# Performance work log

Measured on AMD Instinct MI355X. Metric: run time of the kernel, lower is better.

The kernel has to match this reference:

```python
import jax, jax.numpy as jnp
import numpy as np

EPS = 1e-8


def kabsch_align(P, Q):
    """Align P to Q per the original torch code. P, Q: [B, N, 3].

    Note: the torch code unpacks torch.linalg.svd as (U, S, V) where the third
    return is actually Vh; we faithfully reproduce that exact math.
    """
    P_mean = jnp.mean(P, axis=1, keepdims=True)          # [B,1,3]
    Q_mean = jnp.mean(Q, axis=1, keepdims=True)
    P_c = P - P_mean
    Q_c = Q - Q_mean
    H = jnp.einsum('bni,bnj->bij', P_c, Q_c)             # [B,3,3] covariance
    U, S, Vh = jnp.linalg.svd(H, full_matrices=False)
    Ut = jnp.swapaxes(U, 1, 2)
    d = jnp.linalg.det(jnp.matmul(Vh, Ut))               # [B]
    e = jnp.stack([jnp.ones_like(d), jnp.ones_like(d), d], axis=-1)  # diag(1,1,d)
    R = jnp.einsum('bik,bk,bkj->bij', Vh, e, Ut)         # [B,3,3]
    # P_aligned = P_c @ R^T + Q_mean
    return jnp.einsum('bni,bji->bnj', P_c, R) + Q_mean


def setup_inputs() -> dict:
    key = jax.random.key(0)
    k1, k2 = jax.random.split(key)
    B, K, N = 256, 5, 4096
    preds = jax.random.normal(k1, (B, K, N, 3), dtype=jnp.float32)
    target = jax.random.normal(k2, (B, N, 3), dtype=jnp.float32)
    return {"preds": preds, "target": target}


def reference(preds, target):
    B, K, N, _ = preds.shape
    P = preds.reshape(B * K, N, 3)
    Q = jnp.broadcast_to(target[:, None], (B, K, N, 3)).reshape(B * K, N, 3)
    aligned = kabsch_align(P, Q)                         # [B*K, N, 3]
    mse = jnp.mean((aligned - Q) ** 2, axis=(1, 2))      # [B*K]
    rmsd = jnp.sqrt(mse + EPS).reshape(B, K)
    return jnp.mean(jnp.min(rmsd, axis=1))
```

## Files before the change

kernel.cpp:

```cpp
#include <hip/hip_runtime.h>
#include <math.h>

#define B_    256
#define K_    5
#define N_    4096
#define NPAIR (B_ * K_)
#define NMOM  17

__global__ __launch_bounds__(256) void kabsch_moments(
    const float* __restrict__ preds, const float* __restrict__ target,
    float* __restrict__ mout) {
  const int idx = blockIdx.x;
  const int b = idx & 255;
  const int k = idx >> 8;
  const int pair_orig = b * K_ + k;
  const int tid = threadIdx.x;

  const float4* __restrict__ P4 =
      reinterpret_cast<const float4*>(preds) + (size_t)pair_orig * (N_ * 3 / 4);
  const float4* __restrict__ Q4 =
      reinterpret_cast<const float4*>(target) + (size_t)b * (N_ * 3 / 4);

  float acc[NMOM];
#pragma unroll
  for (int i = 0; i < NMOM; ++i) acc[i] = 0.f;

#pragma unroll
  for (int j = 0; j < 4; ++j) {
    const int c = tid + j * 256;
    const float4 a0 = P4[3 * c + 0], a1 = P4[3 * c + 1], a2 = P4[3 * c + 2];
    const float4 b0 = Q4[3 * c + 0], b1 = Q4[3 * c + 1], b2 = Q4[3 * c + 2];
    const float p[4][3] = {{a0.x, a0.y, a0.z},
                           {a0.w, a1.x, a1.y},
                           {a1.z, a1.w, a2.x},
                           {a2.y, a2.z, a2.w}};
    const float q[4][3] = {{b0.x, b0.y, b0.z},
                           {b0.w, b1.x, b1.y},
                           {b1.z, b1.w, b2.x},
                           {b2.y, b2.z, b2.w}};
#pragma unroll
    for (int m = 0; m < 4; ++m) {
      const float px = p[m][0], py = p[m][1], pz = p[m][2];
      const float qx = q[m][0], qy = q[m][1], qz = q[m][2];
      acc[0] += px; acc[1] += py; acc[2] += pz;
      acc[3] += qx; acc[4] += qy; acc[5] += qz;
      acc[6] = fmaf(px, px, fmaf(py, py, fmaf(pz, pz, acc[6])));
      acc[7] = fmaf(qx, qx, fmaf(qy, qy, fmaf(qz, qz, acc[7])));
      acc[8]  = fmaf(px, qx, acc[8]);
      acc[9]  = fmaf(px, qy, acc[9]);
      acc[10] = fmaf(px, qz, acc[10]);
      acc[11] = fmaf(py, qx, acc[11]);
      acc[12] = fmaf(py, qy, acc[12]);
      acc[13] = fmaf(py, qz, acc[13]);
      acc[14] = fmaf(pz, qx, acc[14]);
      acc[15] = fmaf(pz, qy, acc[15]);
      acc[16] = fmaf(pz, qz, acc[16]);
    }
  }

#pragma unroll
  for (int off = 32; off > 0; off >>= 1) {
#pragma unroll
    for (int i = 0; i < NMOM; ++i) acc[i] += __shfl_down(acc[i], off, 64);
  }

  __shared__ float red[4][NMOM];
  const int lane = tid & 63, wid = tid >> 6;
  if (lane == 0) {
#pragma unroll
    for (int i = 0; i < NMOM; ++i) red[wid][i] = acc[i];
  }
  __syncthreads();
  if (tid < NMOM) {
    mout[(size_t)idx * NMOM + tid] =
        red[0][tid] + red[1][tid] + red[2][tid] + red[3][tid];
  }
}

__device__ inline void cross3(const double* a, const double* b, double* c) {
  c[0] = a[1] * b[2] - a[2] * b[1];
  c[1] = a[2] * b[0] - a[0] * b[2];
  c[2] = a[0] * b[1] - a[1] * b[0];
}
__device__ inline double dot3(const double* a, const double* b) {
  return a[0] * b[0] + a[1] * b[1] + a[2] * b[2];
}
__device__ inline void fixsign3(double* v) {
  const double a0 = fabs(v[0]), a1 = fabs(v[1]), a2 = fabs(v[2]);
  const int i = (a0 >= a1 && a0 >= a2) ? 0 : ((a1 >= a2) ? 1 : 2);
  if (v[i] < 0.0) { v[0] = -v[0]; v[1] = -v[1]; v[2] = -v[2]; }
}
__device__ inline void eigvec3(const double A[3][3], double lam, double* v) {
  const double r0[3] = {A[0][0] - lam, A[0][1], A[0][2]};
  const double r1[3] = {A[1][0], A[1][1] - lam, A[1][2]};
  const double r2[3] = {A[2][0], A[2][1], A[2][2] - lam};
  double c01[3], c02[3], c12[3];
  cross3(r0, r1, c01); cross3(r0, r2, c02); cross3(r1, r2, c12);
  const double n01 = dot3(c01, c01), n02 = dot3(c02, c02), n12 = dot3(c12, c12);
  const double* best = c01; double nb = n01;
  if (n02 > nb) { best = c02; nb = n02; }
  if (n12 > nb) { best = c12; nb = n12; }
  if (nb < 1e-280) { v[0] = 1.0; v[1] = 0.0; v[2] = 0.0; return; }
  const double inv = 1.0 / sqrt(nb);
  v[0] = best[0] * inv; v[1] = best[1] * inv; v[2] = best[2] * inv;
}

__global__ __launch_bounds__(256) void kabsch_svd(
    const float* __restrict__ mo, float* __restrict__ rmsd) {
  const int idx = blockIdx.x * blockDim.x + threadIdx.x;
  if (idx >= NPAIR) return;
  const float* m = mo + (size_t)idx * NMOM;
  const double invN = 1.0 / (double)N_;

  const double sP[3] = {m[0], m[1], m[2]};
  const double sQ[3] = {m[3], m[4], m[5]};
  double H[3][3];
#pragma unroll
  for (int i = 0; i < 3; ++i)
#pragma unroll
    for (int j = 0; j < 3; ++j)
      H[i][j] = (double)m[8 + 3 * i + j] - sP[i] * sQ[j] * invN;

  const double Sp = (double)m[6] - dot3(sP, sP) * invN;
  const double Sq = (double)m[7] - dot3(sQ, sQ) * invN;

  double A[3][3];
#pragma unroll
  for (int i = 0; i < 3; ++i)
#pragma unroll
    for (int j = 0; j < 3; ++j)
      A[i][j] = H[0][i] * H[0][j] + H[1][i] * H[1][j] + H[2][i] * H[2][j];

  double lam[3];
  double V[3][3];
  const double q = (A[0][0] + A[1][1] + A[2][2]) / 3.0;
  const double p1 = A[0][1] * A[0][1] + A[0][2] * A[0][2] + A[1][2] * A[1][2];
  const double p2 = (A[0][0] - q) * (A[0][0] - q) +
                    (A[1][1] - q) * (A[1][1] - q) +
                    (A[2][2] - q) * (A[2][2] - q) + 2.0 * p1;
  if (p2 < 1e-30) {
    lam[0] = lam[1] = lam[2] = q;
#pragma unroll
    for (int i = 0; i < 3; ++i)
#pragma unroll
      for (int j = 0; j < 3; ++j) V[i][j] = (i == j) ? 1.0 : 0.0;
  } else {
    const double p = sqrt(p2 / 6.0);
    const double invp = 1.0 / p;
    double Bm[3][3];
#pragma unroll
    for (int i = 0; i < 3; ++i)
#pragma unroll
      for (int j = 0; j < 3; ++j)
        Bm[i][j] = (A[i][j] - ((i == j) ? q : 0.0)) * invp;
    const double detB =
        Bm[0][0] * (Bm[1][1] * Bm[2][2] - Bm[1][2] * Bm[2][1]) -
        Bm[0][1] * (Bm[1][0] * Bm[2][2] - Bm[1][2] * Bm[2][0]) +
        Bm[0][2] * (Bm[1][0] * Bm[2][1] - Bm[1][1] * Bm[2][0]);
    double r = detB * 0.5;
    r = fmin(1.0, fmax(-1.0, r));
    const double phi = acos(r) / 3.0;
    lam[0] = q + 2.0 * p * cos(phi);
    lam[2] = q + 2.0 * p * cos(phi + 2.0943951023931953);
    lam[1] = 3.0 * q - lam[0] - lam[2];

    double v1[3], v2[3], v3[3];
    eigvec3(A, lam[0], v1);
    eigvec3(A, lam[1], v2);
    const double d12 = dot3(v1, v2);
    v2[0] -= d12 * v1[0]; v2[1] -= d12 * v1[1]; v2[2] -= d12 * v1[2];
    double n2 = dot3(v2, v2);
    if (n2 < 1e-24) {
      const double a0 = fabs(v1[0]), a1f = fabs(v1[1]), a2f = fabs(v1[2]);
      int ax = (a0 <= a1f && a0 <= a2f) ? 0 : ((a1f <= a2f) ? 1 : 2);
      double e[3] = {0.0, 0.0, 0.0};
      e[ax] = 1.0;
      const double de = dot3(v1, e);
      v2[0] = e[0] - de * v1[0]; v2[1] = e[1] - de * v1[1]; v2[2] = e[2] - de * v1[2];
      n2 = dot3(v2, v2);
    }
    const double invn2 = 1.0 / sqrt(n2);
    v2[0] *= invn2; v2[1] *= invn2; v2[2] *= invn2;

    fixsign3(v1);
    fixsign3(v2);
    cross3(v1, v2, v3);
#pragma unroll
    for (int i = 0; i < 3; ++i) { V[i][0] = v1[i]; V[i][1] = v2[i]; V[i][2] = v3[i]; }
  }

  const double S0 = sqrt(fmax(lam[0], 0.0));
  const double S1 = sqrt(fmax(lam[1], 0.0));
  const double S2 = sqrt(fmax(lam[2], 0.0));

  const double detH =
      H[0][0] * (H[1][1] * H[2][2] - H[1][2] * H[2][1]) -
      H[0][1] * (H[1][0] * H[2][2] - H[1][2] * H[2][0]) +
      H[0][2] * (H[1][0] * H[2][1] - H[1][1] * H[2][0]);
  const double dsg = (detH >= 0.0) ? 1.0 : -1.0;

  const double M00 = V[0][0] * V[0][0] + V[1][0] * V[0][1] + V[2][0] * V[0][2];
  const double M11 = V[0][1] * V[1][0] + V[1][1] * V[1][1] + V[2][1] * V[1][2];
  const double M22 = V[0][2] * V[2][0] + V[1][2] * V[2][1] + V[2][2] * V[2][2];

  const double T = S0 * M00 + S1 * M11 + dsg * S2 * M22;
  const double mse = (Sp + Sq - 2.0 * T) / (3.0 * (double)N_);
  rmsd[idx] = (float)sqrt(mse + 1e-8);
}

__global__ __launch_bounds__(256) void kabsch_final(
    const float* __restrict__ rmsd, float* __restrict__ out) {
  const int b = threadIdx.x;
  float mn = rmsd[b];
#pragma unroll
  for (int k = 1; k < K_; ++k) mn = fminf(mn, rmsd[k * 256 + b]);
#pragma unroll
  for (int off = 32; off > 0; off >>= 1) mn += __shfl_down(mn, off, 64);
  __shared__ float s[4];
  if ((b & 63) == 0) s[b >> 6] = mn;
  __syncthreads();
  if (b == 0) out[0] = (s[0] + s[1] + s[2] + s[3]) * (1.0f / 256.0f);
}

extern "C" void kernel_launch(void* const* d_in, const int* in_sizes, int n_in,
                              void* d_out, int out_size, void* d_ws, size_t ws_size,
                              hipStream_t stream) {
  const float* preds = (const float*)d_in[0];
  const float* target = (const float*)d_in[1];
  float* out = (float*)d_out;
  float* mo = (float*)d_ws;
  float* rm = mo + (size_t)NPAIR * NMOM;

  hipLaunchKernelGGL(kabsch_moments, dim3(NPAIR), dim3(256), 0, stream,
                     preds, target, mo);
  hipLaunchKernelGGL(kabsch_svd, dim3((NPAIR + 255) / 256), dim3(256), 0, stream,
                     mo, rm);
  hipLaunchKernelGGL(kabsch_final, dim3(1), dim3(256), 0, stream, rm, out);
}
```

Baseline: 23.46 us.

## Fuse moments, SVD and final reduction into one kernel with last-block pattern

Merges the three kernels into a single launch. Each block reduces its moments, thread 0 computes the per-pair SVD-based RMSD in double precision and publishes it, and an atomic counter lets the last block do the min-over-K and mean reduction. This removes two kernel launches and the moments round-trip through global memory. In exchange it adds a memset launch for the counter and puts a serial double-precision eigen-solve on one thread at the tail of every block.

```diff
diff --git a/kernel.cpp b/kernel.cpp
--- a/kernel.cpp
+++ b/kernel.cpp
@@ -7,9 +7,136 @@
 #define NPAIR (B_ * K_)
 #define NMOM  17
 
-__global__ __launch_bounds__(256) void kabsch_moments(
+__device__ inline void cross3(const double* a, const double* b, double* c) {
+  c[0] = a[1] * b[2] - a[2] * b[1];
+  c[1] = a[2] * b[0] - a[0] * b[2];
+  c[2] = a[0] * b[1] - a[1] * b[0];
+}
+__device__ inline double dot3(const double* a, const double* b) {
+  return a[0] * b[0] + a[1] * b[1] + a[2] * b[2];
+}
+__device__ inline void fixsign3(double* v) {
+  const double a0 = fabs(v[0]), a1 = fabs(v[1]), a2 = fabs(v[2]);
+  const int i = (a0 >= a1 && a0 >= a2) ? 0 : ((a1 >= a2) ? 1 : 2);
+  if (v[i] < 0.0) { v[0] = -v[0]; v[1] = -v[1]; v[2] = -v[2]; }
+}
+__device__ inline void eigvec3(const double A[3][3], double lam, double* v) {
+  const double r0[3] = {A[0][0] - lam, A[0][1], A[0][2]};
+  const double r1[3] = {A[1][0], A[1][1] - lam, A[1][2]};
+  const double r2[3] = {A[2][0], A[2][1], A[2][2] - lam};
+  double c01[3], c02[3], c12[3];
+  cross3(r0, r1, c01); cross3(r0, r2, c02); cross3(r1, r2, c12);
+  const double n01 = dot3(c01, c01), n02 = dot3(c02, c02), n12 = dot3(c12, c12);
+  const double* best = c01; double nb = n01;
+  if (n02 > nb) { best = c02; nb = n02; }
+  if (n12 > nb) { best = c12; nb = n12; }
+  if (nb < 1e-280) { v[0] = 1.0; v[1] = 0.0; v[2] = 0.0; return; }
+  const double inv = 1.0 / sqrt(nb);
+  v[0] = best[0] * inv; v[1] = best[1] * inv; v[2] = best[2] * inv;
+}
+
+__device__ inline float svd_rmsd(const float* m) {
+  const double invN = 1.0 / (double)N_;
+  const double sP[3] = {m[0], m[1], m[2]};
+  const double sQ[3] = {m[3], m[4], m[5]};
+  double H[3][3];
+#pragma unroll
+  for (int i = 0; i < 3; ++i)
+#pragma unroll
+    for (int j = 0; j < 3; ++j)
+      H[i][j] = (double)m[8 + 3 * i + j] - sP[i] * sQ[j] * invN;
+
+  const double Sp = (double)m[6] - dot3(sP, sP) * invN;
+  const double Sq = (double)m[7] - dot3(sQ, sQ) * invN;
+
+  double A[3][3];
+#pragma unroll
+  for (int i = 0; i < 3; ++i)
+#pragma unroll
+    for (int j = 0; j < 3; ++j)
+      A[i][j] = H[0][i] * H[0][j] + H[1][i] * H[1][j] + H[2][i] * H[2][j];
+
+  double lam[3];
+  double V[3][3];
+  const double q = (A[0][0] + A[1][1] + A[2][2]) / 3.0;
+  const double p1 = A[0][1] * A[0][1] + A[0][2] * A[0][2] + A[1][2] * A[1][2];
+  const double p2 = (A[0][0] - q) * (A[0][0] - q) +
+                    (A[1][1] - q) * (A[1][1] - q) +
+                    (A[2][2] - q) * (A[2][2] - q) + 2.0 * p1;
+  if (p2 < 1e-30) {
+    lam[0] = lam[1] = lam[2] = q;
+#pragma unroll
+    for (int i = 0; i < 3; ++i)
+#pragma unroll
+      for (int j = 0; j < 3; ++j) V[i][j] = (i == j) ? 1.0 : 0.0;
+  } else {
+    const double p = sqrt(p2 / 6.0);
+    const double invp = 1.0 / p;
+    double Bm[3][3];
+#pragma unroll
+    for (int i = 0; i < 3; ++i)
+#pragma unroll
+      for (int j = 0; j < 3; ++j)
+        Bm[i][j] = (A[i][j] - ((i == j) ? q : 0.0)) * invp;
+    const double detB =
+        Bm[0][0] * (Bm[1][1] * Bm[2][2] - Bm[1][2] * Bm[2][1]) -
+        Bm[0][1] * (Bm[1][0] * Bm[2][2] - Bm[1][2] * Bm[2][0]) +
+        Bm[0][2] * (Bm[1][0] * Bm[2][1] - Bm[1][1] * Bm[2][0]);
+    double r = detB * 0.5;
+    r = fmin(1.0, fmax(-1.0, r));
+    const double phi = acos(r) / 3.0;
+    lam[0] = q + 2.0 * p * cos(phi);
+    lam[2] = q + 2.0 * p * cos(phi + 2.0943951023931953);
+    lam[1] = 3.0 * q - lam[0] - lam[2];
+
+    double v1[3], v2[3], v3[3];
+    eigvec3(A, lam[0], v1);
+    eigvec3(A, lam[1], v2);
+    const double d12 = dot3(v1, v2);
+    v2[0] -= d12 * v1[0]; v2[1] -= d12 * v1[1]; v2[2] -= d12 * v1[2];
+    double n2 = dot3(v2, v2);
+    if (n2 < 1e-24) {
+      const double a0 = fabs(v1[0]), a1f = fabs(v1[1]), a2f = fabs(v1[2]);
+      int ax = (a0 <= a1f && a0 <= a2f) ? 0 : ((a1f <= a2f) ? 1 : 2);
+      double e[3] = {0.0, 0.0, 0.0};
+      e[ax] = 1.0;
+      const double de = dot3(v1, e);
+      v2[0] = e[0] - de * v1[0]; v2[1] = e[1] - de * v1[1]; v2[2] = e[2] - de * v1[2];
+      n2 = dot3(v2, v2);
+    }
+    const double invn2 = 1.0 / sqrt(n2);
+    v2[0] *= invn2; v2[1] *= invn2; v2[2] *= invn2;
+
+    fixsign3(v1);
+    fixsign3(v2);
+    cross3(v1, v2, v3);
+#pragma unroll
+    for (int i = 0; i < 3; ++i) { V[i][0] = v1[i]; V[i][1] = v2[i]; V[i][2] = v3[i]; }
+  }
+
+  const double S0 = sqrt(fmax(lam[0], 0.0));
+  const double S1 = sqrt(fmax(lam[1], 0.0));
+  const double S2 = sqrt(fmax(lam[2], 0.0));
+
+  const double detH =
+      H[0][0] * (H[1][1] * H[2][2] - H[1][2] * H[2][1]) -
+      H[0][1] * (H[1][0] * H[2][2] - H[1][2] * H[2][0]) +
+      H[0][2] * (H[1][0] * H[2][1] - H[1][1] * H[2][0]);
+  const double dsg = (detH >= 0.0) ? 1.0 : -1.0;
+
+  const double M00 = V[0][0] * V[0][0] + V[1][0] * V[0][1] + V[2][0] * V[0][2];
+  const double M11 = V[0][1] * V[1][0] + V[1][1] * V[1][1] + V[2][1] * V[1][2];
+  const double M22 = V[0][2] * V[2][0] + V[1][2] * V[2][1] + V[2][2] * V[2][2];
+
+  const double T = S0 * M00 + S1 * M11 + dsg * S2 * M22;
+  const double mse = (Sp + Sq - 2.0 * T) / (3.0 * (double)N_);
+  return (float)sqrt(mse + 1e-8);
+}
+
+__global__ __launch_bounds__(256) void kabsch_fused(
     const float* __restrict__ preds, const float* __restrict__ target,
-    float* __restrict__ mout) {
+    unsigned int* __restrict__ cnt, float* __restrict__ rm,
+    float* __restrict__ out) {
   const int idx = blockIdx.x;
   const int b = idx & 255;
   const int k = idx >> 8;
@@ -65,161 +192,45 @@
   }
 
   __shared__ float red[4][NMOM];
+  __shared__ unsigned int s_done;
   const int lane = tid & 63, wid = tid >> 6;
   if (lane == 0) {
 #pragma unroll
     for (int i = 0; i < NMOM; ++i) red[wid][i] = acc[i];
   }
   __syncthreads();
-  if (tid < NMOM) {
-    mout[(size_t)idx * NMOM + tid] =
-        red[0][tid] + red[1][tid] + red[2][tid] + red[3][tid];
-  }
-}
-
-__device__ inline void cross3(const double* a, const double* b, double* c) {
-  c[0] = a[1] * b[2] - a[2] * b[1];
-  c[1] = a[2] * b[0] - a[0] * b[2];
-  c[2] = a[0] * b[1] - a[1] * b[0];
-}
-__device__ inline double dot3(const double* a, const double* b) {
-  return a[0] * b[0] + a[1] * b[1] + a[2] * b[2];
-}
-__device__ inline void fixsign3(double* v) {
-  const double a0 = fabs(v[0]), a1 = fabs(v[1]), a2 = fabs(v[2]);
-  const int i = (a0 >= a1 && a0 >= a2) ? 0 : ((a1 >= a2) ? 1 : 2);
-  if (v[i] < 0.0) { v[0] = -v[0]; v[1] = -v[1]; v[2] = -v[2]; }
-}
-__device__ inline void eigvec3(const double A[3][3], double lam, double* v) {
-  const double r0[3] = {A[0][0] - lam, A[0][1], A[0][2]};
-  const double r1[3] = {A[1][0], A[1][1] - lam, A[1][2]};
-  const double r2[3] = {A[2][0], A[2][1], A[2][2] - lam};
-  double c01[3], c02[3], c12[3];
-  cross3(r0, r1, c01); cross3(r0, r2, c02); cross3(r1, r2, c12);
-  const double n01 = dot3(c01, c01), n02 = dot3(c02, c02), n12 = dot3(c12, c12);
-  const double* best = c01; double nb = n01;
-  if (n02 > nb) { best = c02; nb = n02; }
-  if (n12 > nb) { best = c12; nb = n12; }
-  if (nb < 1e-280) { v[0] = 1.0; v[1] = 0.0; v[2] = 0.0; return; }
-  const double inv = 1.0 / sqrt(nb);
-  v[0] = best[0] * inv; v[1] = best[1] * inv; v[2] = best[2] * inv;
-}
-
-__global__ __launch_bounds__(256) void kabsch_svd(
-    const float* __restrict__ mo, float* __restrict__ rmsd) {
-  const int idx = blockIdx.x * blockDim.x + threadIdx.x;
-  if (idx >= NPAIR) return;
-  const float* m = mo + (size_t)idx * NMOM;
-  const double invN = 1.0 / (double)N_;
-
-  const double sP[3] = {m[0], m[1], m[2]};
-  const double sQ[3] = {m[3], m[4], m[5]};
-  double H[3][3];
-#pragma unroll
-  for (int i = 0; i < 3; ++i)
-#pragma unroll
-    for (int j = 0; j < 3; ++j)
-      H[i][j] = (double)m[8 + 3 * i + j] - sP[i] * sQ[j] * invN;
-
-  const double Sp = (double)m[6] - dot3(sP, sP) * invN;
-  const double Sq = (double)m[7] - dot3(sQ, sQ) * invN;
-
-  double A[3][3];
-#pragma unroll
-  for (int i = 0; i < 3; ++i)
-#pragma unroll
-    for (int j = 0; j < 3; ++j)
-      A[i][j] = H[0][i] * H[0][j] + H[1][i] * H[1][j] + H[2][i] * H[2][j];
-
-  double lam[3];
-  double V[3][3];
-  const double q = (A[0][0] + A[1][1] + A[2][2]) / 3.0;
-  const double p1 = A[0][1] * A[0][1] + A[0][2] * A[0][2] + A[1][2] * A[1][2];
-  const double p2 = (A[0][0] - q) * (A[0][0] - q) +
-                    (A[1][1] - q) * (A[1][1] - q) +
-                    (A[2][2] - q) * (A[2][2] - q) + 2.0 * p1;
-  if (p2 < 1e-30) {
-    lam[0] = lam[1] = lam[2] = q;
-#pragma unroll
-    for (int i = 0; i < 3; ++i)
-#pragma unroll
-      for (int j = 0; j < 3; ++j) V[i][j] = (i == j) ? 1.0 : 0.0;
-  } else {
-    const double p = sqrt(p2 / 6.0);
-    const double invp = 1.0 / p;
-    double Bm[3][3];
-#pragma unroll
-    for (int i = 0; i < 3; ++i)
-#pragma unroll
-      for (int j = 0; j < 3; ++j)
-        Bm[i][j] = (A[i][j] - ((i == j) ? q : 0.0)) * invp;
-    const double detB =
-        Bm[0][0] * (Bm[1][1] * Bm[2][2] - Bm[1][2] * Bm[2][1]) -
-        Bm[0][1] * (Bm[1][0] * Bm[2][2] - Bm[1][2] * Bm[2][0]) +
-        Bm[0][2] * (Bm[1][0] * Bm[2][1] - Bm[1][1] * Bm[2][0]);
-    double r = detB * 0.5;
-    r = fmin(1.0, fmax(-1.0, r));
-    const double phi = acos(r) / 3.0;
-    lam[0] = q + 2.0 * p * cos(phi);
-    lam[2] = q + 2.0 * p * cos(phi + 2.0943951023931953);
-    lam[1] = 3.0 * q - lam[0] - lam[2];
-
-    double v1[3], v2[3], v3[3];
-    eigvec3(A, lam[0], v1);
-    eigvec3(A, lam[1], v2);
-    const double d12 = dot3(v1, v2);
-    v2[0] -= d12 * v1[0]; v2[1] -= d12 * v1[1]; v2[2] -= d12 * v1[2];
-    double n2 = dot3(v2, v2);
-    if (n2 < 1e-24) {
-      const double a0 = fabs(v1[0]), a1f = fabs(v1[1]), a2f = fabs(v1[2]);
-      int ax = (a0 <= a1f && a0 <= a2f) ? 0 : ((a1f <= a2f) ? 1 : 2);
-      double e[3] = {0.0, 0.0, 0.0};
-      e[ax] = 1.0;
-      const double de = dot3(v1, e);
-      v2[0] = e[0] - de * v1[0]; v2[1] = e[1] - de * v1[1]; v2[2] = e[2] - de * v1[2];
-      n2 = dot3(v2, v2);
+
+  if (tid == 0) {
+    float m[NMOM];
+#pragma unroll
+    for (int i = 0; i < NMOM; ++i)
+      m[i] = red[0][i] + red[1][i] + red[2][i] + red[3][i];
+    const float r = svd_rmsd(m);
+    __hip_atomic_store(rm + idx, r, __ATOMIC_RELAXED, __HIP_MEMORY_SCOPE_AGENT);
+    const unsigned int old = __hip_atomic_fetch_add(
+        cnt, 1u, __ATOMIC_ACQ_REL, __HIP_MEMORY_SCOPE_AGENT);
+    s_done = (old == (unsigned int)(NPAIR - 1)) ? 1u : 0u;
+  }
+  __syncthreads();
+
+  if (s_done) {
+    __threadfence();
+    const int bb = tid;
+    float mn = __hip_atomic_load(rm + bb, __ATOMIC_RELAXED,
+                                 __HIP_MEMORY_SCOPE_AGENT);
+#pragma unroll
+    for (int kk = 1; kk < K_; ++kk) {
+      const float v = __hip_atomic_load(rm + kk * 256 + bb, __ATOMIC_RELAXED,
+                                        __HIP_MEMORY_SCOPE_AGENT);
+      mn = fminf(mn, v);
     }
-    const double invn2 = 1.0 / sqrt(n2);
-    v2[0] *= invn2; v2[1] *= invn2; v2[2] *= invn2;
-
-    fixsign3(v1);
-    fixsign3(v2);
-    cross3(v1, v2, v3);
-#pragma unroll
-    for (int i = 0; i < 3; ++i) { V[i][0] = v1[i]; V[i][1] = v2[i]; V[i][2] = v3[i]; }
-  }
-
-  const double S0 = sqrt(fmax(lam[0], 0.0));
-  const double S1 = sqrt(fmax(lam[1], 0.0));
-  const double S2 = sqrt(fmax(lam[2], 0.0));
-
-  const double detH =
-      H[0][0] * (H[1][1] * H[2][2] - H[1][2] * H[2][1]) -
-      H[0][1] * (H[1][0] * H[2][2] - H[1][2] * H[2][0]) +
-      H[0][2] * (H[1][0] * H[2][1] - H[1][1] * H[2][0]);
-  const double dsg = (detH >= 0.0) ? 1.0 : -1.0;
-
-  const double M00 = V[0][0] * V[0][0] + V[1][0] * V[0][1] + V[2][0] * V[0][2];
-  const double M11 = V[0][1] * V[1][0] + V[1][1] * V[1][1] + V[2][1] * V[1][2];
-  const double M22 = V[0][2] * V[2][0] + V[1][2] * V[2][1] + V[2][2] * V[2][2];
-
-  const double T = S0 * M00 + S1 * M11 + dsg * S2 * M22;
-  const double mse = (Sp + Sq - 2.0 * T) / (3.0 * (double)N_);
-  rmsd[idx] = (float)sqrt(mse + 1e-8);
-}
-
-__global__ __launch_bounds__(256) void kabsch_final(
-    const float* __restrict__ rmsd, float* __restrict__ out) {
-  const int b = threadIdx.x;
-  float mn = rmsd[b];
-#pragma unroll
-  for (int k = 1; k < K_; ++k) mn = fminf(mn, rmsd[k * 256 + b]);
-#pragma unroll
-  for (int off = 32; off > 0; off >>= 1) mn += __shfl_down(mn, off, 64);
-  __shared__ float s[4];
-  if ((b & 63) == 0) s[b >> 6] = mn;
-  __syncthreads();
-  if (b == 0) out[0] = (s[0] + s[1] + s[2] + s[3]) * (1.0f / 256.0f);
+#pragma unroll
+    for (int off = 32; off > 0; off >>= 1) mn += __shfl_down(mn, off, 64);
+    __shared__ float s[4];
+    if ((tid & 63) == 0) s[tid >> 6] = mn;
+    __syncthreads();
+    if (tid == 0) out[0] = (s[0] + s[1] + s[2] + s[3]) * (1.0f / 256.0f);
+  }
 }
 
 extern "C" void kernel_launch(void* const* d_in, const int* in_sizes, int n_in,
@@ -228,12 +239,10 @@
   const float* preds = (const float*)d_in[0];
   const float* target = (const float*)d_in[1];
   float* out = (float*)d_out;
-  float* mo = (float*)d_ws;
-  float* rm = mo + (size_t)NPAIR * NMOM;
-
-  hipLaunchKernelGGL(kabsch_moments, dim3(NPAIR), dim3(256), 0, stream,
-                     preds, target, mo);
-  hipLaunchKernelGGL(kabsch_svd, dim3((NPAIR + 255) / 256), dim3(256), 0, stream,
-                     mo, rm);
-  hipLaunchKernelGGL(kabsch_final, dim3(1), dim3(256), 0, stream, rm, out);
-}
+  unsigned int* cnt = (unsigned int*)d_ws;
+  float* rm = (float*)d_ws + 4;
+
+  hipMemsetAsync(d_ws, 0, 4, stream);
+  hipLaunchKernelGGL(kabsch_fused, dim3(NPAIR), dim3(256), 0, stream,
+                     preds, target, cnt, rm, out);
+}
```

New measurement: 49.88 us. 2.13x slower.
